# Performance work log

Hardware: AMD Instinct MI355X
Metric: run time of the kernel (lower is better)

## Reference

```python
import jax, jax.numpy as jnp
import numpy as np
from jax import lax

N_CLASSES = 10
N_EXPERTS = 45  # 10 choose 2
EPS = 1e-5

# lookup table: (i1, i2) with i1 < i2 -> flat expert id (matches nested loop order)
_tbl = np.zeros((N_CLASSES, N_CLASSES), dtype=np.int32)
_k = 0
for _i1 in range(N_CLASSES):
    for _i2 in range(_i1 + 1, N_CLASSES):
        _tbl[_i1, _i2] = _k
        _k += 1
PAIR_TABLE = jnp.asarray(_tbl)


def _downscale(x):
    # AvgPool2d(3, stride=3) on 28x28 -> 9x9 (floor: uses top-left 27x27)
    B = x.shape[0]
    return x[:, :, :27, :27].reshape(B, 1, 9, 3, 9, 3).mean(axis=(3, 5))


def _bn_eval(h, gamma, beta, mean, var):
    scale = gamma * lax.rsqrt(var + EPS)
    return h * scale[None, :, None, None] + (beta - mean * scale)[None, :, None, None]


def _stage1(x, w1, b1, g1, be1, m1, v1, fcw1, fcb1):
    xd = _downscale(x)                                         # [B,1,9,9]
    h = lax.conv_general_dilated(xd, w1, (1, 1), 'VALID',
                                 dimension_numbers=('NCHW', 'OIHW', 'NCHW'))
    h = h + b1[None, :, None, None]                            # [B,20,7,7]
    h = _bn_eval(h, g1, be1, m1, v1)
    h = jax.nn.relu(h)
    B = h.shape[0]
    h = h[:, :, :6, :6].reshape(B, 20, 3, 2, 3, 2).max(axis=(3, 5))  # maxpool2 -> [B,20,3,3]
    h = h.reshape(B, 180)
    return h @ fcw1.T + fcb1                                   # [B,10] raw logits


def reference(x, w1, b1, g1, be1, m1, v1, fcw1, fcb1,
              w2, b2, g2, be2, m2, v2, fcw2, fcb2):
    B = x.shape[0]
    logits1 = _stage1(x, w1, b1, g1, be1, m1, v1, fcw1, fcb1)  # [B,10]
    ls1 = jax.nn.log_softmax(logits1, axis=1)

    # routing: top-2 class indices, sorted ascending, -> pairwise expert id
    top2 = jnp.sort(jnp.argsort(ls1, axis=1)[:, -2:], axis=1)  # [B,2]
    idx0, idx1 = top2[:, 0], top2[:, 1]
    eid = PAIR_TABLE[idx0, idx1]                               # [B]

    # stage 2 (TinyNet2) with per-example gathered expert params
    xd = _downscale(x)                                         # [B,1,9,9]
    # extract 5x5 conv patches (valid, stride 1): output spatial 5x5
    patches = jnp.stack([xd[:, 0, i:i + 5, j:j + 5]
                         for i in range(5) for j in range(5)], axis=1)  # [B,25,5,5]
    Wsel = w2.reshape(N_EXPERTS, 15, 25)[eid]                  # [B,15,25]
    h = jnp.einsum('bkhw,bok->bohw', patches, Wsel) + b2[eid][:, :, None, None]  # [B,15,5,5]
    scale = (g2 * lax.rsqrt(v2 + EPS))[eid]                    # [B,15]
    shift = (be2 - m2 * g2 * lax.rsqrt(v2 + EPS))[eid]
    h = h * scale[:, :, None, None] + shift[:, :, None, None]
    h = jax.nn.relu(h)
    h = h[:, :, :4, :4].reshape(B, 15, 2, 2, 2, 2).max(axis=(3, 5))  # [B,15,2,2]
    feat = h.reshape(B, 60)
    s2 = jnp.einsum('bf,bof->bo', feat, fcw2[eid]) + fcb2[eid]  # [B,2]

    # combine: scatter the two expert logits into the routed columns
    rows = jnp.arange(B)
    out = jnp.full((B, N_CLASSES), -100.0, dtype=logits1.dtype)
    out = out.at[rows, idx0].set(s2[:, 0]).at[rows, idx1].set(s2[:, 1])
    # eval-mode bypass: use stage1 raw logits if max log-prob > 0.3
    use1 = jnp.max(ls1, axis=1) > 0.3
    out = jnp.where(use1[:, None], logits1, out)
    out = jax.nn.log_softmax(out, axis=1)
    return (logits1, out)


def setup_inputs() -> dict:
    key = jax.random.key(0)
    ks = jax.random.split(key, 18)
    B = 65536
    s = 0.1
    return {
        'x': jax.random.normal(ks[0], (B, 1, 28, 28), dtype=jnp.float32),
        # stage1 (TinyNet, 20 kernels, k=3)
        'w1': jax.random.normal(ks[1], (20, 1, 3, 3), dtype=jnp.float32) * s,
        'b1': jax.random.normal(ks[2], (20,), dtype=jnp.float32) * s,
        'g1': jax.random.normal(ks[3], (20,), dtype=jnp.float32) * s + 1.0,
        'be1': jax.random.normal(ks[4], (20,), dtype=jnp.float32) * s,
        'm1': jax.random.normal(ks[5], (20,), dtype=jnp.float32) * s,
        'v1': jax.random.uniform(ks[6], (20,), dtype=jnp.float32) + 0.5,
        'fcw1': jax.random.normal(ks[7], (10, 180), dtype=jnp.float32) * s,
        'fcb1': jax.random.normal(ks[8], (10,), dtype=jnp.float32) * s,
        # 45 stacked stage2 experts (TinyNet2, 15 kernels, k=5)
        'w2': jax.random.normal(ks[9], (45, 15, 1, 5, 5), dtype=jnp.float32) * s,
        'b2': jax.random.normal(ks[10], (45, 15), dtype=jnp.float32) * s,
        'g2': jax.random.normal(ks[11], (45, 15), dtype=jnp.float32) * s + 1.0,
        'be2': jax.random.normal(ks[12], (45, 15), dtype=jnp.float32) * s,
        'm2': jax.random.normal(ks[13], (45, 15), dtype=jnp.float32) * s,
        'v2': jax.random.uniform(ks[14], (45, 15), dtype=jnp.float32) + 0.5,
        'fcw2': jax.random.normal(ks[15], (45, 2, 60), dtype=jnp.float32) * s,
        'fcb2': jax.random.normal(ks[16], (45, 2), dtype=jnp.float32) * s,
    }
```

## Files before the change

### kernel.cpp

```cpp
#include <hip/hip_runtime.h>
#include <cmath>

#define EPSF 1e-5f

#define OFF_B2F   18900
#define OFF_FC2   19576
#define OFF_FCB2  24976
#define OFF_W1P   25068
#define OFF_FCW1R 25308
#define OFF_B1F   27468

__global__ __launch_bounds__(256) void setup_tables(
    const float* __restrict__ w1, const float* __restrict__ b1,
    const float* __restrict__ g1, const float* __restrict__ be1,
    const float* __restrict__ m1, const float* __restrict__ v1,
    const float* __restrict__ w2, const float* __restrict__ b2,
    const float* __restrict__ g2, const float* __restrict__ be2,
    const float* __restrict__ m2, const float* __restrict__ v2,
    const float* __restrict__ fcw2, const float* __restrict__ fcb2,
    const float* __restrict__ fcw1,
    float* __restrict__ ws)
{
  const int t  = blockIdx.x * blockDim.x + threadIdx.x;
  const int nt = gridDim.x * blockDim.x;
  float* W2F   = ws;
  float* B2F   = ws + OFF_B2F;
  float* FC2   = ws + OFF_FC2;
  float* FCB2  = ws + OFF_FCB2;
  float* W1P   = ws + OFF_W1P;
  float* FCW1R = ws + OFF_FCW1R;
  float* B1F   = ws + OFF_B1F;

  for (int idx = t; idx < 18900; idx += nt) {
    int kk = idx & 3, rest = idx >> 2;
    int e = rest % 45, ok4 = rest / 45;
    int k4 = ok4 % 7, o = ok4 / 7;
    int k = k4 * 4 + kk;
    float s = g2[e*15+o] / sqrtf(v2[e*15+o] + EPSF);
    W2F[idx] = (k < 25) ? w2[(e*15+o)*25 + k] * s : 0.0f;
  }
  for (int idx = t; idx < 675; idx += nt) {
    int e = idx % 45, o = idx / 45;
    float s = g2[e*15+o] / sqrtf(v2[e*15+o] + EPSF);
    B2F[idx] = b2[e*15+o]*s + be2[e*15+o] - m2[e*15+o]*s;
  }
  for (int idx = t; idx < 5400; idx += nt) {
    int kk = idx & 3, rest = idx >> 2;
    int e = rest % 45, t2 = rest / 45;
    int f4 = t2 % 15, oo = t2 / 15;
    FC2[idx] = fcw2[(e*2+oo)*60 + f4*4 + kk];
  }
  for (int idx = t; idx < 90; idx += nt) {
    int e = idx % 45, oo = idx / 45;
    FCB2[idx] = fcb2[e*2+oo];
  }
  for (int idx = t; idx < 240; idx += nt) {
    int j = idx % 12, ch = idx / 12;
    float s = g1[ch] / sqrtf(v1[ch] + EPSF);
    W1P[idx] = (j < 9) ? w1[ch*9 + j] * s : 0.0f;
  }
  for (int idx = t; idx < 2160; idx += nt) {
    int c = idx % 12, r2 = idx / 12;
    int pp = r2 % 9, ch = r2 / 9;
    FCW1R[idx] = (c < 10) ? fcw1[c*180 + ch*9 + pp] : 0.0f;
  }
  for (int idx = t; idx < 20; idx += nt) {
    float s = g1[idx] / sqrtf(v1[idx] + EPSF);
    B1F[idx] = b1[idx]*s + be1[idx] - m1[idx]*s;
  }
}

#define GETC(arr, k) ((k)%4==0 ? arr[(k)/4].x : (k)%4==1 ? arr[(k)/4].y : \
                      (k)%4==2 ? arr[(k)/4].z : arr[(k)/4].w)

__global__ __launch_bounds__(256, 3) void fused_k(
    const float* __restrict__ x,
    const float* __restrict__ ws,
    const float* __restrict__ fcb1,
    float* __restrict__ out, int B)
{
  __shared__ float xds[64 * 68];

  const int t  = threadIdx.x;
  const int p  = t & 3;
  const int sl = t >> 2;
  const int b  = blockIdx.x * 64 + sl;
  const bool valid = (b < B);

  const float* W2F   = ws;
  const float* B2F   = ws + OFF_B2F;
  const float* FC2   = ws + OFF_FC2;
  const float* FCB2  = ws + OFF_FCB2;
  const float* W1P   = ws + OFF_W1P;
  const float* FCW1R = ws + OFF_FCW1R;
  const float* B1F   = ws + OFF_B1F;

  if (valid) {
    const float* xb = x + (size_t)b * 784;
    #pragma unroll
    for (int ri = 0; ri < 2; ri++) {
      const int r = 2*p + ri;
      float4 rowv[3][6];
      #pragma unroll
      for (int dr = 0; dr < 3; dr++) {
        const float4* rv = reinterpret_cast<const float4*>(xb + (3*r + dr) * 28);
        #pragma unroll
        for (int q = 0; q < 6; q++) rowv[dr][q] = rv[q];
      }
      float d[8];
      #pragma unroll
      for (int c = 0; c < 8; c++) {
        float s = 0.0f;
        #pragma unroll
        for (int dr = 0; dr < 3; dr++)
          s += GETC(rowv[dr], 3*c) + GETC(rowv[dr], 3*c+1) + GETC(rowv[dr], 3*c+2);
        d[c] = s * (1.0f / 9.0f);
      }
      float4* dst = reinterpret_cast<float4*>(&xds[sl*68 + r*8]);
      dst[0] = make_float4(d[0], d[1], d[2], d[3]);
      dst[1] = make_float4(d[4], d[5], d[6], d[7]);
    }
  }
  __syncthreads();

  float xd[64];
  #pragma unroll
  for (int r = 0; r < 8; r++) {
    const float4* src = reinterpret_cast<const float4*>(&xds[sl*68 + r*8]);
    float4 a = src[0], bq = src[1];
    xd[r*8+0]=a.x;  xd[r*8+1]=a.y;  xd[r*8+2]=a.z;  xd[r*8+3]=a.w;
    xd[r*8+4]=bq.x; xd[r*8+5]=bq.y; xd[r*8+6]=bq.z; xd[r*8+7]=bq.w;
  }

  float logits[10];
  #pragma unroll
  for (int c = 0; c < 10; c++) logits[c] = 0.0f;

  #pragma unroll 1
  for (int ci = 0; ci < 5; ci++) {
    const int ch = p*5 + ci;
    const float4* wp = reinterpret_cast<const float4*>(W1P + ch*12);
    float4 w0 = wp[0], w1v = wp[1], w2v = wp[2];
    const float w_[9] = {w0.x,w0.y,w0.z,w0.w,w1v.x,w1v.y,w1v.z,w1v.w,w2v.x};
    const float bb = B1F[ch];
    float feat[9];
    #pragma unroll
    for (int pr = 0; pr < 3; pr++) {
      #pragma unroll
      for (int pc = 0; pc < 3; pc++) {
        float c00 = bb, c01 = bb, c10 = bb, c11 = bb;
        #pragma unroll
        for (int dr = 0; dr < 3; dr++) {
          #pragma unroll
          for (int dc = 0; dc < 3; dc++) {
            float wk = w_[dr*3 + dc];
            c00 = fmaf(xd[(2*pr+0+dr)*8 + 2*pc+0+dc], wk, c00);
            c01 = fmaf(xd[(2*pr+0+dr)*8 + 2*pc+1+dc], wk, c01);
            c10 = fmaf(xd[(2*pr+1+dr)*8 + 2*pc+0+dc], wk, c10);
            c11 = fmaf(xd[(2*pr+1+dr)*8 + 2*pc+1+dc], wk, c11);
          }
        }
        feat[pr*3+pc] = fmaxf(fmaxf(fmaxf(c00, c01), fmaxf(c10, c11)), 0.0f);
      }
    }
    #pragma unroll
    for (int pp = 0; pp < 9; pp++) {
      const float4* f4 = reinterpret_cast<const float4*>(FCW1R + (ch*9 + pp)*12);
      float4 f0 = f4[0], f1 = f4[1], f2 = f4[2];
      const float fv = feat[pp];
      logits[0] = fmaf(fv, f0.x, logits[0]);
      logits[1] = fmaf(fv, f0.y, logits[1]);
      logits[2] = fmaf(fv, f0.z, logits[2]);
      logits[3] = fmaf(fv, f0.w, logits[3]);
      logits[4] = fmaf(fv, f1.x, logits[4]);
      logits[5] = fmaf(fv, f1.y, logits[5]);
      logits[6] = fmaf(fv, f1.z, logits[6]);
      logits[7] = fmaf(fv, f1.w, logits[7]);
      logits[8] = fmaf(fv, f2.x, logits[8]);
      logits[9] = fmaf(fv, f2.y, logits[9]);
    }
  }

  #pragma unroll
  for (int c = 0; c < 10; c++) {
    float v = logits[c];
    v += __shfl_xor(v, 1);
    v += __shfl_xor(v, 2);
    logits[c] = v + fcb1[c];
  }

  int i1 = 0; float v1m = logits[0];
  #pragma unroll
  for (int c = 1; c < 10; c++) { if (logits[c] >= v1m) { v1m = logits[c]; i1 = c; } }
  int i2 = 0; float v2m = -3.0e38f;
  #pragma unroll
  for (int c = 0; c < 10; c++) { if (c != i1 && logits[c] >= v2m) { v2m = logits[c]; i2 = c; } }
  const int idx0 = i1 < i2 ? i1 : i2;
  const int idx1 = i1 < i2 ? i2 : i1;
  int eid = 8*idx0 - (idx0*(idx0-1))/2 + idx1 - 1;
  eid = eid < 0 ? 0 : (eid > 44 ? 44 : eid);

  float sume = 0.0f;
  #pragma unroll
  for (int c = 0; c < 10; c++) sume += expf(logits[c] - v1m);
  const bool use1 = (-logf(sume)) > 0.3f;

  const float4* W2F4 = reinterpret_cast<const float4*>(W2F);
  const float4* FC24 = reinterpret_cast<const float4*>(FC2);
  float s2a = 0.0f, s2b = 0.0f;

  #pragma unroll 1
  for (int oi = 0; oi < 4; oi++) {
    const int o = p + 4*oi;
    if (o < 15) {
      float4 wv[7];
      #pragma unroll
      for (int k4 = 0; k4 < 7; k4++) wv[k4] = W2F4[(o*7 + k4)*45 + eid];
      const float bias = B2F[o*45 + eid];
      const float4 fa = FC24[o*45 + eid];
      const float4 fb = FC24[(15 + o)*45 + eid];
      float feat0 = 0.f, feat1 = 0.f, feat2 = 0.f, feat3 = 0.f;
      #pragma unroll
      for (int ph = 0; ph < 2; ph++) {
        #pragma unroll
        for (int pw = 0; pw < 2; pw++) {
          float c00 = bias, c01 = bias, c10 = bias, c11 = bias;
          #pragma unroll
          for (int i = 0; i < 5; i++) {
            #pragma unroll
            for (int j = 0; j < 5; j++) {
              float wk = GETC(wv, i*5 + j);
              c00 = fmaf(xd[(2*ph+0+i)*8 + 2*pw+0+j], wk, c00);
              c01 = fmaf(xd[(2*ph+0+i)*8 + 2*pw+1+j], wk, c01);
              c10 = fmaf(xd[(2*ph+1+i)*8 + 2*pw+0+j], wk, c10);
              c11 = fmaf(xd[(2*ph+1+i)*8 + 2*pw+1+j], wk, c11);
            }
          }
          float f = fmaxf(fmaxf(fmaxf(c00, c01), fmaxf(c10, c11)), 0.0f);
          if (ph == 0 && pw == 0) feat0 = f;
          else if (ph == 0)       feat1 = f;
          else if (pw == 0)       feat2 = f;
          else                    feat3 = f;
        }
      }
      s2a = fmaf(feat0, fa.x, fmaf(feat1, fa.y, fmaf(feat2, fa.z, fmaf(feat3, fa.w, s2a))));
      s2b = fmaf(feat0, fb.x, fmaf(feat1, fb.y, fmaf(feat2, fb.z, fmaf(feat3, fb.w, s2b))));
    }
  }
  s2a += __shfl_xor(s2a, 1); s2a += __shfl_xor(s2a, 2);
  s2b += __shfl_xor(s2b, 1); s2b += __shfl_xor(s2b, 2);
  s2a += FCB2[eid];
  s2b += FCB2[45 + eid];

  float o10[10];
  #pragma unroll
  for (int c = 0; c < 10; c++) {
    float v = -100.0f;
    v = (c == idx0) ? s2a : v;
    v = (c == idx1) ? s2b : v;
    o10[c] = use1 ? logits[c] : v;
  }
  float m2x = o10[0];
  #pragma unroll
  for (int c = 1; c < 10; c++) m2x = fmaxf(m2x, o10[c]);
  float se2 = 0.0f;
  #pragma unroll
  for (int c = 0; c < 10; c++) se2 += expf(o10[c] - m2x);
  const float lse2 = m2x + logf(se2);

  if (valid) {
    const size_t base = (size_t)b * 10;
    if (p == 0) {
      #pragma unroll
      for (int c = 0; c < 5; c++) out[base + c] = logits[c];
    } else if (p == 1) {
      #pragma unroll
      for (int c = 5; c < 10; c++) out[base + c] = logits[c];
    } else if (p == 2) {
      #pragma unroll
      for (int c = 0; c < 5; c++) out[(size_t)B*10 + base + c] = o10[c] - lse2;
    } else {
      #pragma unroll
      for (int c = 5; c < 10; c++) out[(size_t)B*10 + base + c] = o10[c] - lse2;
    }
  }
}

extern "C" void kernel_launch(void* const* d_in, const int* in_sizes, int n_in,
                              void* d_out, int out_size, void* d_ws, size_t ws_size,
                              hipStream_t stream) {
  const float* x    = (const float*)d_in[0];
  const float* w1   = (const float*)d_in[1];
  const float* b1   = (const float*)d_in[2];
  const float* g1   = (const float*)d_in[3];
  const float* be1  = (const float*)d_in[4];
  const float* m1   = (const float*)d_in[5];
  const float* v1   = (const float*)d_in[6];
  const float* fcw1 = (const float*)d_in[7];
  const float* fcb1 = (const float*)d_in[8];
  const float* w2   = (const float*)d_in[9];
  const float* b2   = (const float*)d_in[10];
  const float* g2   = (const float*)d_in[11];
  const float* be2  = (const float*)d_in[12];
  const float* m2   = (const float*)d_in[13];
  const float* v2   = (const float*)d_in[14];
  const float* fcw2 = (const float*)d_in[15];
  const float* fcb2 = (const float*)d_in[16];
  float* out = (float*)d_out;
  float* ws  = (float*)d_ws;
  const int B = in_sizes[0] / 784;

  setup_tables<<<80, 256, 0, stream>>>(w1, b1, g1, be1, m1, v1,
                                       w2, b2, g2, be2, m2, v2, fcw2, fcb2, fcw1, ws);
  fused_k<<<(B + 63)/64, 256, 0, stream>>>(x, ws, fcb1, out, B);
}
```

Before: 376.7 us.

## Stage small weight tables in LDS and coalesce output stores via shared memory

Packs the small stage-1 weights, biases and stage-2 bias tables into one contiguous 4096-float image in setup. Each block copies that image into LDS with float4 loads, so the per-thread scattered global reads become shared-memory reads. Outputs are staged in LDS and written back as coalesced float4 stores for full blocks. The change also switches to fast __expf/__logf and replaces the occupancy hint with waves_per_eu. In exchange it needs much more LDS per block (about 33KB) and extra barriers, which may lower occupancy, and the fast math intrinsics may differ slightly in precision.

```diff
diff --git a/kernel.cpp b/kernel.cpp
--- a/kernel.cpp
+++ b/kernel.cpp
@@ -3,12 +3,15 @@
 
 #define EPSF 1e-5f
 
-#define OFF_B2F   18900
 #define OFF_FC2   19576
-#define OFF_FCB2  24976
-#define OFF_W1P   25068
-#define OFF_FCW1R 25308
-#define OFF_B1F   27468
+#define OFF_IMG   25088
+
+#define I_W1P    0
+#define I_FCW1R  240
+#define I_B1F    2400
+#define I_FCB1   2420
+#define I_B2F    2432
+#define I_FCB2   3108
 
 __global__ __launch_bounds__(256) void setup_tables(
     const float* __restrict__ w1, const float* __restrict__ b1,
@@ -18,18 +21,14 @@
     const float* __restrict__ g2, const float* __restrict__ be2,
     const float* __restrict__ m2, const float* __restrict__ v2,
     const float* __restrict__ fcw2, const float* __restrict__ fcb2,
-    const float* __restrict__ fcw1,
+    const float* __restrict__ fcw1, const float* __restrict__ fcb1,
     float* __restrict__ ws)
 {
   const int t  = blockIdx.x * blockDim.x + threadIdx.x;
   const int nt = gridDim.x * blockDim.x;
-  float* W2F   = ws;
-  float* B2F   = ws + OFF_B2F;
-  float* FC2   = ws + OFF_FC2;
-  float* FCB2  = ws + OFF_FCB2;
-  float* W1P   = ws + OFF_W1P;
-  float* FCW1R = ws + OFF_FCW1R;
-  float* B1F   = ws + OFF_B1F;
+  float* W2F = ws;
+  float* FC2 = ws + OFF_FC2;
+  float* IMG = ws + OFF_IMG;
 
   for (int idx = t; idx < 18900; idx += nt) {
     int kk = idx & 3, rest = idx >> 2;
@@ -39,47 +38,61 @@
     float s = g2[e*15+o] / sqrtf(v2[e*15+o] + EPSF);
     W2F[idx] = (k < 25) ? w2[(e*15+o)*25 + k] * s : 0.0f;
   }
-  for (int idx = t; idx < 675; idx += nt) {
-    int e = idx % 45, o = idx / 45;
-    float s = g2[e*15+o] / sqrtf(v2[e*15+o] + EPSF);
-    B2F[idx] = b2[e*15+o]*s + be2[e*15+o] - m2[e*15+o]*s;
-  }
   for (int idx = t; idx < 5400; idx += nt) {
     int kk = idx & 3, rest = idx >> 2;
     int e = rest % 45, t2 = rest / 45;
     int f4 = t2 % 15, oo = t2 / 15;
     FC2[idx] = fcw2[(e*2+oo)*60 + f4*4 + kk];
   }
-  for (int idx = t; idx < 90; idx += nt) {
-    int e = idx % 45, oo = idx / 45;
-    FCB2[idx] = fcb2[e*2+oo];
-  }
-  for (int idx = t; idx < 240; idx += nt) {
-    int j = idx % 12, ch = idx / 12;
-    float s = g1[ch] / sqrtf(v1[ch] + EPSF);
-    W1P[idx] = (j < 9) ? w1[ch*9 + j] * s : 0.0f;
-  }
-  for (int idx = t; idx < 2160; idx += nt) {
-    int c = idx % 12, r2 = idx / 12;
-    int pp = r2 % 9, ch = r2 / 9;
-    FCW1R[idx] = (c < 10) ? fcw1[c*180 + ch*9 + pp] : 0.0f;
-  }
-  for (int idx = t; idx < 20; idx += nt) {
-    float s = g1[idx] / sqrtf(v1[idx] + EPSF);
-    B1F[idx] = b1[idx]*s + be1[idx] - m1[idx]*s;
+  for (int i = t; i < 4096; i += nt) {
+    float v = 0.0f;
+    if (i < I_FCW1R) {
+      int ch = i / 12, j = i % 12;
+      if (j < 9) {
+        float s = g1[ch] / sqrtf(v1[ch] + EPSF);
+        v = w1[ch*9 + j] * s;
+      }
+    } else if (i < I_B1F) {
+      int k = i - I_FCW1R;
+      int c = k % 12, r2 = k / 12, pp = r2 % 9, ch = r2 / 9;
+      if (c < 10) v = fcw1[c*180 + ch*9 + pp];
+    } else if (i < I_FCB1) {
+      int ch = i - I_B1F;
+      float s = g1[ch] / sqrtf(v1[ch] + EPSF);
+      v = b1[ch]*s + be1[ch] - m1[ch]*s;
+    } else if (i < I_B2F) {
+      int k = i - I_FCB1;
+      if (k < 10) v = fcb1[k];
+    } else if (i < I_FCB2) {
+      int k = i - I_B2F;
+      if (k < 675) {
+        int e = k % 45, o = k / 45;
+        float s = g2[e*15+o] / sqrtf(v2[e*15+o] + EPSF);
+        v = b2[e*15+o]*s + be2[e*15+o] - m2[e*15+o]*s;
+      }
+    } else {
+      int k = i - I_FCB2;
+      if (k < 90) {
+        int e = k % 45, oo = k / 45;
+        v = fcb2[e*2+oo];
+      }
+    }
+    IMG[i] = v;
   }
 }
 
 #define GETC(arr, k) ((k)%4==0 ? arr[(k)/4].x : (k)%4==1 ? arr[(k)/4].y : \
                       (k)%4==2 ? arr[(k)/4].z : arr[(k)/4].w)
 
-__global__ __launch_bounds__(256, 3) void fused_k(
+#define T_TAB 4352
+
+__global__ __attribute__((amdgpu_waves_per_eu(2, 4))) __launch_bounds__(256)
+void fused_k(
     const float* __restrict__ x,
     const float* __restrict__ ws,
-    const float* __restrict__ fcb1,
     float* __restrict__ out, int B)
 {
-  __shared__ float xds[64 * 68];
+  __shared__ float lds[8448];
 
   const int t  = threadIdx.x;
   const int p  = t & 3;
@@ -87,13 +100,8 @@
   const int b  = blockIdx.x * 64 + sl;
   const bool valid = (b < B);
 
-  const float* W2F   = ws;
-  const float* B2F   = ws + OFF_B2F;
-  const float* FC2   = ws + OFF_FC2;
-  const float* FCB2  = ws + OFF_FCB2;
-  const float* W1P   = ws + OFF_W1P;
-  const float* FCW1R = ws + OFF_FCW1R;
-  const float* B1F   = ws + OFF_B1F;
+  const float4* img4 = reinterpret_cast<const float4*>(ws + OFF_IMG);
+  float4 tv0 = img4[t], tv1 = img4[t + 256], tv2 = img4[t + 512], tv3 = img4[t + 768];
 
   if (valid) {
     const float* xb = x + (size_t)b * 784;
@@ -116,17 +124,21 @@
           s += GETC(rowv[dr], 3*c) + GETC(rowv[dr], 3*c+1) + GETC(rowv[dr], 3*c+2);
         d[c] = s * (1.0f / 9.0f);
       }
-      float4* dst = reinterpret_cast<float4*>(&xds[sl*68 + r*8]);
+      float4* dst = reinterpret_cast<float4*>(&lds[sl*68 + r*8]);
       dst[0] = make_float4(d[0], d[1], d[2], d[3]);
       dst[1] = make_float4(d[4], d[5], d[6], d[7]);
     }
   }
+  {
+    float4* tab4 = reinterpret_cast<float4*>(&lds[T_TAB]);
+    tab4[t] = tv0; tab4[t + 256] = tv1; tab4[t + 512] = tv2; tab4[t + 768] = tv3;
+  }
   __syncthreads();
 
   float xd[64];
   #pragma unroll
   for (int r = 0; r < 8; r++) {
-    const float4* src = reinterpret_cast<const float4*>(&xds[sl*68 + r*8]);
+    const float4* src = reinterpret_cast<const float4*>(&lds[sl*68 + r*8]);
     float4 a = src[0], bq = src[1];
     xd[r*8+0]=a.x;  xd[r*8+1]=a.y;  xd[r*8+2]=a.z;  xd[r*8+3]=a.w;
     xd[r*8+4]=bq.x; xd[r*8+5]=bq.y; xd[r*8+6]=bq.z; xd[r*8+7]=bq.w;
@@ -139,10 +151,10 @@
   #pragma unroll 1
   for (int ci = 0; ci < 5; ci++) {
     const int ch = p*5 + ci;
-    const float4* wp = reinterpret_cast<const float4*>(W1P + ch*12);
+    const float4* wp = reinterpret_cast<const float4*>(&lds[T_TAB + I_W1P + ch*12]);
     float4 w0 = wp[0], w1v = wp[1], w2v = wp[2];
     const float w_[9] = {w0.x,w0.y,w0.z,w0.w,w1v.x,w1v.y,w1v.z,w1v.w,w2v.x};
-    const float bb = B1F[ch];
+    const float bb = lds[T_TAB + I_B1F + ch];
     float feat[9];
     #pragma unroll
     for (int pr = 0; pr < 3; pr++) {
@@ -165,7 +177,7 @@
     }
     #pragma unroll
     for (int pp = 0; pp < 9; pp++) {
-      const float4* f4 = reinterpret_cast<const float4*>(FCW1R + (ch*9 + pp)*12);
+      const float4* f4 = reinterpret_cast<const float4*>(&lds[T_TAB + I_FCW1R + (ch*9 + pp)*12]);
       float4 f0 = f4[0], f1 = f4[1], f2 = f4[2];
       const float fv = feat[pp];
       logits[0] = fmaf(fv, f0.x, logits[0]);
@@ -186,7 +198,7 @@
     float v = logits[c];
     v += __shfl_xor(v, 1);
     v += __shfl_xor(v, 2);
-    logits[c] = v + fcb1[c];
+    logits[c] = v + lds[T_TAB + I_FCB1 + c];
   }
 
   int i1 = 0; float v1m = logits[0];
@@ -202,11 +214,20 @@
 
   float sume = 0.0f;
   #pragma unroll
-  for (int c = 0; c < 10; c++) sume += expf(logits[c] - v1m);
-  const bool use1 = (-logf(sume)) > 0.3f;
-
-  const float4* W2F4 = reinterpret_cast<const float4*>(W2F);
-  const float4* FC24 = reinterpret_cast<const float4*>(FC2);
+  for (int c = 0; c < 10; c++) sume += __expf(logits[c] - v1m);
+  const bool use1 = (-__logf(sume)) > 0.3f;
+
+  __syncthreads();
+  if (p == 0) {
+    #pragma unroll
+    for (int c = 0; c < 5; c++) lds[sl*10 + c] = logits[c];
+  } else if (p == 1) {
+    #pragma unroll
+    for (int c = 5; c < 10; c++) lds[sl*10 + c] = logits[c];
+  }
+
+  const float4* W2F4 = reinterpret_cast<const float4*>(ws);
+  const float4* FC24 = reinterpret_cast<const float4*>(ws + OFF_FC2);
   float s2a = 0.0f, s2b = 0.0f;
 
   #pragma unroll 1
@@ -216,7 +237,7 @@
       float4 wv[7];
       #pragma unroll
       for (int k4 = 0; k4 < 7; k4++) wv[k4] = W2F4[(o*7 + k4)*45 + eid];
-      const float bias = B2F[o*45 + eid];
+      const float bias = lds[T_TAB + I_B2F + o*45 + eid];
       const float4 fa = FC24[o*45 + eid];
       const float4 fb = FC24[(15 + o)*45 + eid];
       float feat0 = 0.f, feat1 = 0.f, feat2 = 0.f, feat3 = 0.f;
@@ -249,39 +270,56 @@
   }
   s2a += __shfl_xor(s2a, 1); s2a += __shfl_xor(s2a, 2);
   s2b += __shfl_xor(s2b, 1); s2b += __shfl_xor(s2b, 2);
-  s2a += FCB2[eid];
-  s2b += FCB2[45 + eid];
-
+  s2a += lds[T_TAB + I_FCB2 + eid];
+  s2b += lds[T_TAB + I_FCB2 + 45 + eid];
+
+  __syncthreads();
   float o10[10];
   #pragma unroll
   for (int c = 0; c < 10; c++) {
     float v = -100.0f;
     v = (c == idx0) ? s2a : v;
     v = (c == idx1) ? s2b : v;
-    o10[c] = use1 ? logits[c] : v;
+    o10[c] = use1 ? lds[sl*10 + c] : v;
   }
   float m2x = o10[0];
   #pragma unroll
   for (int c = 1; c < 10; c++) m2x = fmaxf(m2x, o10[c]);
   float se2 = 0.0f;
   #pragma unroll
-  for (int c = 0; c < 10; c++) se2 += expf(o10[c] - m2x);
-  const float lse2 = m2x + logf(se2);
-
-  if (valid) {
+  for (int c = 0; c < 10; c++) se2 += __expf(o10[c] - m2x);
+  const float lse2 = m2x + __logf(se2);
+
+  if (p == 2) {
+    #pragma unroll
+    for (int c = 0; c < 5; c++) lds[640 + sl*10 + c] = o10[c] - lse2;
+  } else if (p == 3) {
+    #pragma unroll
+    for (int c = 5; c < 10; c++) lds[640 + sl*10 + c] = o10[c] - lse2;
+  }
+  __syncthreads();
+
+  if (blockIdx.x * 64 + 64 <= B) {
+    const float4* l4 = reinterpret_cast<const float4*>(lds);
+    const size_t o1 = (size_t)blockIdx.x * 640;
+    if (t < 160)
+      *reinterpret_cast<float4*>(out + o1 + (size_t)t*4) = l4[t];
+    if (t >= 96)
+      *reinterpret_cast<float4*>(out + (size_t)B*10 + o1 + (size_t)(t-96)*4) = l4[160 + (t-96)];
+  } else if (valid) {
     const size_t base = (size_t)b * 10;
     if (p == 0) {
       #pragma unroll
-      for (int c = 0; c < 5; c++) out[base + c] = logits[c];
+      for (int c = 0; c < 5; c++) out[base + c] = lds[sl*10 + c];
     } else if (p == 1) {
       #pragma unroll
-      for (int c = 5; c < 10; c++) out[base + c] = logits[c];
+      for (int c = 5; c < 10; c++) out[base + c] = lds[sl*10 + c];
     } else if (p == 2) {
       #pragma unroll
-      for (int c = 0; c < 5; c++) out[(size_t)B*10 + base + c] = o10[c] - lse2;
+      for (int c = 0; c < 5; c++) out[(size_t)B*10 + base + c] = lds[640 + sl*10 + c];
     } else {
       #pragma unroll
-      for (int c = 5; c < 10; c++) out[(size_t)B*10 + base + c] = o10[c] - lse2;
+      for (int c = 5; c < 10; c++) out[(size_t)B*10 + base + c] = lds[640 + sl*10 + c];
     }
   }
 }
@@ -311,6 +349,7 @@
   const int B = in_sizes[0] / 784;
 
   setup_tables<<<80, 256, 0, stream>>>(w1, b1, g1, be1, m1, v1,
-                                       w2, b2, g2, be2, m2, v2, fcw2, fcb2, fcw1, ws);
-  fused_k<<<(B + 63)/64, 256, 0, stream>>>(x, ws, fcb1, out, B);
+                                       w2, b2, g2, be2, m2, v2,
+                                       fcw2, fcb2, fcw1, fcb1, ws);
+  fused_k<<<(B + 63)/64, 256, 0, stream>>>(x, ws, out, B);
 }
```

After: 334.4 us. 1.13x faster.
